# Optimization experiments

Hardware: AMD Instinct MI355X
Metric: run time of the kernel (lower is better)

The kernel has to match this reference:

```python
import jax, jax.numpy as jnp
from jax import lax
import numpy as np
import math

# Static module config (matches init_kwargs)
K = 5            # kernel_size
MD = 3           # max_degree
HH = (MD + 1) ** 2   # n_harmonics = 16
CIN, F = 16, 32
B, D = 1, 48
NJ = K // 2      # n_radial_profiles (one shell per integer radius 1..K//2)
DN = ('NCDHW', 'OIDHW', 'NCDHW')


def _sh_table(ct, st, phi):
    """Complex spherical harmonics Y_n^m up to degree 3 (Condon-Shortley), [*grid, HH]."""
    fourpi = 4.0 * np.pi
    def N(n, m):
        return np.sqrt((2 * n + 1) / fourpi * math.factorial(n - m) / math.factorial(n + m))
    P = {
        (0, 0): np.ones_like(ct),
        (1, 0): ct,
        (1, 1): -st,
        (2, 0): 0.5 * (3 * ct ** 2 - 1),
        (2, 1): -3.0 * ct * st,
        (2, 2): 3.0 * st ** 2,
        (3, 0): 0.5 * (5 * ct ** 3 - 3 * ct),
        (3, 1): -1.5 * (5 * ct ** 2 - 1) * st,
        (3, 2): 15.0 * ct * st ** 2,
        (3, 3): -15.0 * st ** 3,
    }
    sh = np.zeros(ct.shape + (HH,), dtype=np.complex64)
    for n in range(MD + 1):
        for m in range(0, n + 1):
            y = (N(n, m) * P[(n, m)]).astype(np.complex64) * np.exp(1j * m * phi).astype(np.complex64)
            sh[..., n * n + n + m] = y
            if m > 0:
                sh[..., n * n + n - m] = ((-1) ** m) * np.conj(y)
    return sh


def _make_atoms():
    """Radial-shell x SH atoms: [K,K,K,NJ,HH] complex, L2-normalized per atom."""
    g = np.linspace(-(K // 2), K // 2, K)
    x, y, z = np.meshgrid(g, g, g, indexing='xy')
    r = np.sqrt(x * x + y * y + z * z)
    phi = np.arctan2(y, x)
    ct = np.divide(z, r, out=np.zeros_like(r), where=r != 0)
    st = np.sqrt(np.clip(1.0 - ct * ct, 0.0, None))
    sh = _sh_table(ct, st, phi)                                     # [K,K,K,HH]
    prof = np.stack([np.clip(1.0 - np.abs(r - j), 0.0, None) for j in range(1, NJ + 1)], -1)  # [K,K,K,NJ]
    atoms = prof[..., :, None] * sh[..., None, :]                   # [K,K,K,NJ,HH]
    norm = np.sqrt((np.abs(atoms) ** 2).sum(axis=(0, 1, 2), keepdims=True))
    atoms = atoms / np.where(norm > 0, norm, 1.0)
    return atoms.real.astype(np.float32), atoms.imag.astype(np.float32)


ATOMS_R, ATOMS_I = _make_atoms()
DEG = np.repeat(np.arange(MD + 1), 2 * np.arange(MD + 1) + 1)       # harmonic index -> degree (len HH)


def setup_inputs() -> dict:
    key = jax.random.key(0)
    ks = jax.random.split(key, 4)
    lim = float(np.sqrt(6.0 / (CIN + F)))
    return {
        'x': jax.random.normal(ks[0], (B, CIN, D, D, D), jnp.float32),
        'w': jax.random.uniform(ks[1], (CIN, F, NJ, MD + 1), jnp.float32, -lim, lim),
        'central_w': jax.random.uniform(ks[2], (F, CIN, 1, 1, 1), jnp.float32, -lim, lim),
        'central_b': jnp.zeros((F,), jnp.float32),
        'spec_bias': jnp.zeros(((MD + 1) * F,), jnp.float32),
        'proj_w': jax.random.uniform(ks[3], (F, (MD + 1) * F, 1, 1, 1), jnp.float32, -0.1, 0.1),
        'proj_b': jnp.zeros((F,), jnp.float32),
    }


def _forward(x, w, central_w, central_b, spec_bias, proj_w, proj_b):
    # Expand per-degree weights to per-harmonic (repeat_interleave over 2n+1 orders),
    # then fuse the per-channel SH conv + channel/radial weighted sum into a single
    # dense conv with composed kernels (same math as the torch loop + sum over axes 4,6).
    wh = w[..., DEG]                                                 # [C,F,NJ,HH]
    kr = jnp.einsum('cfjh,xyzjh->fhcxyz', wh, jnp.asarray(ATOMS_R)).reshape(F * HH, CIN, K, K, K)
    ki = jnp.einsum('cfjh,xyzjh->fhcxyz', wh, jnp.asarray(ATOMS_I)).reshape(F * HH, CIN, K, K, K)
    yr = lax.conv_general_dilated(x, kr, (1, 1, 1), 'SAME', dimension_numbers=DN)
    yi = lax.conv_general_dilated(x, ki, (1, 1, 1), 'SAME', dimension_numbers=DN)
    b, _, d, h, wd = yr.shape
    yr = yr.reshape(b, F, HH, d, h, wd)
    yi = yi.reshape(b, F, HH, d, h, wd)
    # 1x1x1 central-pixel conv added to the degree-0 (harmonic 0) real map
    cp = lax.conv_general_dilated(x, central_w, (1, 1, 1), 'SAME', dimension_numbers=DN)
    cp = cp + central_b[None, :, None, None, None]
    yr = yr.at[:, :, 0].add(cp)
    # rotation-invariant power spectrum per degree: 1/(2n+1) * sum_m (re^2 + im^2)
    p = yr * yr + yi * yi                                            # [B,F,HH,d,h,w]
    spec = jnp.stack([p[:, :, n * n:n * n + 2 * n + 1].sum(2) / (2 * n + 1) for n in range(MD + 1)], 2)
    spec = spec.reshape(b, F * (MD + 1), d, h, wd) + spec_bias[None, :, None, None, None]
    # activation=('Linear',...) is identity; projection 1x1x1 conv + ReLU
    out = lax.conv_general_dilated(spec, proj_w, (1, 1, 1), 'SAME', dimension_numbers=DN)
    out = out + proj_b[None, :, None, None, None]
    return jax.nn.relu(out)


def reference(x, w, central_w, central_b, spec_bias, proj_w, proj_b):
    return _forward(x, w, central_w, central_b, spec_bias, proj_w, proj_b)
```

## Files before the change

### kernel.cpp

```cpp
#include <hip/hip_runtime.h>
#include <hip/hip_fp16.h>
#include <math.h>


#define TX 8
#define TY 4
#define TZ 4
#define LXX 12
#define LYY 8
#define LZZ 8
#define NPOS 768
#define CPAD 24
#define POSB 48

#define ATAB2_B 0
#define WT2_B   23552
#define CW2_B   31744
#define PWT_B   32768
#define OB_B    49152
#define ED_B    49280

typedef __half2 h2;
union I4H { int4 v; h2 h[4]; };

__global__ __launch_bounds__(256) void ssh_init(
    const float* __restrict__ w, const float* __restrict__ cw,
    const float* __restrict__ proj_w, const float* __restrict__ spec_bias,
    const float* __restrict__ proj_b, char* __restrict__ wsb)
{
    __shared__ float shr[125][16];
    __shared__ float shi[125][16];
    __shared__ float prof[125][2];
    __shared__ float norms[2][16];
    __shared__ int epos[92];
    const int tid = threadIdx.x;
    const float fourpi = 4.0f * 3.14159265358979323846f;

    for (int p = tid; p < 125; p += 256) {
        int d2 = p % 5, d1 = (p / 5) % 5, d0 = p / 25;
        float xc = (float)(d1 - 2), yc = (float)(d0 - 2), zc = (float)(d2 - 2);
        float r2 = xc*xc + yc*yc + zc*zc;
        float r  = sqrtf(r2);
        float phi = atan2f(yc, xc);
        float ct = (r > 0.f) ? (zc / r) : 0.f;
        float st = sqrtf(fmaxf(0.f, 1.f - ct*ct));
        float c1 = cosf(phi), s1 = sinf(phi);
        float c2 = c1*c1 - s1*s1, s2 = 2.f*s1*c1;
        float c3 = c2*c1 - s2*s1, s3 = s2*c1 + c2*s1;
        float P10 = ct,              P11 = -st;
        float P20 = 0.5f*(3.f*ct*ct - 1.f), P21 = -3.f*ct*st, P22 = 3.f*st*st;
        float P30 = 0.5f*(5.f*ct*ct*ct - 3.f*ct);
        float P31 = -1.5f*(5.f*ct*ct - 1.f)*st;
        float P32 = 15.f*ct*st*st;
        float P33 = -15.f*st*st*st;
        float N00 = sqrtf(1.f/fourpi);
        float N10 = sqrtf(3.f/fourpi);
        float N11 = sqrtf(3.f/fourpi * 0.5f);
        float N20 = sqrtf(5.f/fourpi);
        float N21 = sqrtf(5.f/fourpi / 6.f);
        float N22 = sqrtf(5.f/fourpi / 24.f);
        float N30 = sqrtf(7.f/fourpi);
        float N31 = sqrtf(7.f/fourpi / 12.f);
        float N32 = sqrtf(7.f/fourpi / 120.f);
        float N33 = sqrtf(7.f/fourpi / 720.f);
        float b;
        shr[p][0] = N00;               shi[p][0] = 0.f;
        shr[p][2] = N10*P10;           shi[p][2] = 0.f;
        b = N11*P11;
        shr[p][3] =  b*c1;             shi[p][3] =  b*s1;
        shr[p][1] = -b*c1;             shi[p][1] =  b*s1;
        shr[p][6] = N20*P20;           shi[p][6] = 0.f;
        b = N21*P21;
        shr[p][7] =  b*c1;             shi[p][7] =  b*s1;
        shr[p][5] = -b*c1;             shi[p][5] =  b*s1;
        b = N22*P22;
        shr[p][8] =  b*c2;             shi[p][8] =  b*s2;
        shr[p][4] =  b*c2;             shi[p][4] = -b*s2;
        shr[p][12] = N30*P30;          shi[p][12] = 0.f;
        b = N31*P31;
        shr[p][13] =  b*c1;            shi[p][13] =  b*s1;
        shr[p][11] = -b*c1;            shi[p][11] =  b*s1;
        b = N32*P32;
        shr[p][14] =  b*c2;            shi[p][14] =  b*s2;
        shr[p][10] =  b*c2;            shi[p][10] = -b*s2;
        b = N33*P33;
        shr[p][15] =  b*c3;            shi[p][15] =  b*s3;
        shr[p][9]  = -b*c3;            shi[p][9]  =  b*s3;
        prof[p][0] = fmaxf(0.f, 1.f - fabsf(r - 1.f));
        prof[p][1] = fmaxf(0.f, 1.f - fabsf(r - 2.f));
    }
    __syncthreads();

    if (tid < 32) {
        int j = tid >> 4, h = tid & 15;
        float acc = 0.f;
        for (int p = 0; p < 125; ++p) {
            float pr = prof[p][j];
            acc += pr*pr*(shr[p][h]*shr[p][h] + shi[p][h]*shi[p][h]);
        }
        float nn = sqrtf(acc);
        norms[j][h] = (nn > 0.f) ? nn : 1.f;
    }
    if (tid < 125) {
        int p = tid;
        int d2 = p % 5, d1 = (p / 5) % 5, d0 = p / 25;
        int ix = d1 - 2, iy = d0 - 2, iz = d2 - 2;
        int r2i = ix*ix + iy*iy + iz*iz;
        int cls = (r2i == 1) ? 0 : (r2i == 2 || r2i == 3) ? 1
                : (r2i == 4 || r2i == 5 || r2i == 6 || r2i == 8) ? 2 : -1;
        if (cls >= 0) {
            int rank = (cls == 0) ? 0 : (cls == 1) ? 6 : 26;
            for (int q = 0; q < p; ++q) {
                int e2 = q % 5, e1 = (q / 5) % 5, e0 = q / 25;
                int jx = e1 - 2, jy = e0 - 2, jz = e2 - 2;
                int s2i = jx*jx + jy*jy + jz*jz;
                int c2i = (s2i == 1) ? 0 : (s2i == 2 || s2i == 3) ? 1
                       : (s2i == 4 || s2i == 5 || s2i == 6 || s2i == 8) ? 2 : -1;
                rank += (c2i == cls) ? 1 : 0;
            }
            epos[rank] = p;
            ((int*)(wsb + ED_B))[rank] = (d0*(LYY*LXX) + d1*LXX + d2) * POSB;
        }
    }
    __syncthreads();

    h2* at2 = (h2*)(wsb + ATAB2_B);
    for (int t = tid; t < 92*16; t += 256) {
        int e = t >> 4, h = t & 15;
        int p = epos[e];
        float c0 = prof[p][0] / norms[0][h];
        float c1v = prof[p][1] / norms[1][h];
        at2[(h*92+e)*4 + 0] = __float2half2_rn(c0*shr[p][h]);
        at2[(h*92+e)*4 + 1] = __float2half2_rn(c0*shi[p][h]);
        at2[(h*92+e)*4 + 2] = __float2half2_rn(c1v*shr[p][h]);
        at2[(h*92+e)*4 + 3] = __float2half2_rn(c1v*shi[p][h]);
    }
    h2* wt2h = (h2*)(wsb + WT2_B);
    for (int t = tid; t < 2048; t += 256) {
        int n = t >> 9, f = (t >> 4) & 31, j = (t >> 3) & 1, cp = t & 7;
        float a = w[((2*cp*32 + f)*2 + j)*4 + n];
        float b = w[(((2*cp+1)*32 + f)*2 + j)*4 + n];
        wt2h[t] = __halves2half2(__float2half(a), __float2half(b));
    }
    h2* cw2h = (h2*)(wsb + CW2_B);
    for (int t = tid; t < 256; t += 256) {
        int f = t >> 3, cp = t & 7;
        cw2h[t] = __halves2half2(__float2half(cw[f*16 + 2*cp]),
                                 __float2half(cw[f*16 + 2*cp + 1]));
    }
    float* pwT = (float*)(wsb + PWT_B);
    for (int t = tid; t < 4096; t += 256) {
        int i = t >> 5, fo = t & 31;
        pwT[t] = proj_w[fo*128 + i];
    }
    if (tid < 32) {
        float acc = proj_b[tid];
        for (int i = 0; i < 128; ++i) acc += proj_w[tid*128 + i] * spec_bias[i];
        ((float*)(wsb + OB_B))[tid] = acc;
    }
}


__device__ __forceinline__ void conv2c(const __half* __restrict__ ldsh, int baseb,
    const int4* __restrict__ aA, const int4* __restrict__ aB,
    const int* __restrict__ ed, h2 (&zA)[4][8], h2 (&zB)[4][8])
{
#pragma unroll
    for (int r = 0; r < 4; ++r)
#pragma unroll
        for (int q = 0; q < 8; ++q) { zA[r][q] = __float2half2_rn(0.f); zB[r][q] = __float2half2_rn(0.f); }

#pragma unroll 2
    for (int e = 0; e < 6; ++e) {
        I4H ca, cb_, x0, x1;
        ca.v = aA[e]; cb_.v = aB[e];
        const int4* p = (const int4*)((const char*)ldsh + baseb + ed[e]);
        x0.v = p[0]; x1.v = p[1];
#pragma unroll
        for (int q = 0; q < 4; ++q) {
            zA[0][q]   = __hfma2(ca.h[0],  x0.h[q], zA[0][q]);
            zA[1][q]   = __hfma2(ca.h[1],  x0.h[q], zA[1][q]);
            zB[0][q]   = __hfma2(cb_.h[0], x0.h[q], zB[0][q]);
            zB[1][q]   = __hfma2(cb_.h[1], x0.h[q], zB[1][q]);
            zA[0][q+4] = __hfma2(ca.h[0],  x1.h[q], zA[0][q+4]);
            zA[1][q+4] = __hfma2(ca.h[1],  x1.h[q], zA[1][q+4]);
            zB[0][q+4] = __hfma2(cb_.h[0], x1.h[q], zB[0][q+4]);
            zB[1][q+4] = __hfma2(cb_.h[1], x1.h[q], zB[1][q+4]);
        }
    }
#pragma unroll 2
    for (int e = 6; e < 26; ++e) {
        I4H ca, cb_, x0, x1;
        ca.v = aA[e]; cb_.v = aB[e];
        const int4* p = (const int4*)((const char*)ldsh + baseb + ed[e]);
        x0.v = p[0]; x1.v = p[1];
#pragma unroll
        for (int q = 0; q < 4; ++q) {
            zA[0][q]   = __hfma2(ca.h[0],  x0.h[q], zA[0][q]);
            zA[1][q]   = __hfma2(ca.h[1],  x0.h[q], zA[1][q]);
            zA[2][q]   = __hfma2(ca.h[2],  x0.h[q], zA[2][q]);
            zA[3][q]   = __hfma2(ca.h[3],  x0.h[q], zA[3][q]);
            zB[0][q]   = __hfma2(cb_.h[0], x0.h[q], zB[0][q]);
            zB[1][q]   = __hfma2(cb_.h[1], x0.h[q], zB[1][q]);
            zB[2][q]   = __hfma2(cb_.h[2], x0.h[q], zB[2][q]);
            zB[3][q]   = __hfma2(cb_.h[3], x0.h[q], zB[3][q]);
            zA[0][q+4] = __hfma2(ca.h[0],  x1.h[q], zA[0][q+4]);
            zA[1][q+4] = __hfma2(ca.h[1],  x1.h[q], zA[1][q+4]);
            zA[2][q+4] = __hfma2(ca.h[2],  x1.h[q], zA[2][q+4]);
            zA[3][q+4] = __hfma2(ca.h[3],  x1.h[q], zA[3][q+4]);
            zB[0][q+4] = __hfma2(cb_.h[0], x1.h[q], zB[0][q+4]);
            zB[1][q+4] = __hfma2(cb_.h[1], x1.h[q], zB[1][q+4]);
            zB[2][q+4] = __hfma2(cb_.h[2], x1.h[q], zB[2][q+4]);
            zB[3][q+4] = __hfma2(cb_.h[3], x1.h[q], zB[3][q+4]);
        }
    }
#pragma unroll 2
    for (int e = 26; e < 92; ++e) {
        I4H ca, cb_, x0, x1;
        ca.v = aA[e]; cb_.v = aB[e];
        const int4* p = (const int4*)((const char*)ldsh + baseb + ed[e]);
        x0.v = p[0]; x1.v = p[1];
#pragma unroll
        for (int q = 0; q < 4; ++q) {
            zA[2][q]   = __hfma2(ca.h[2],  x0.h[q], zA[2][q]);
            zA[3][q]   = __hfma2(ca.h[3],  x0.h[q], zA[3][q]);
            zB[2][q]   = __hfma2(cb_.h[2], x0.h[q], zB[2][q]);
            zB[3][q]   = __hfma2(cb_.h[3], x0.h[q], zB[3][q]);
            zA[2][q+4] = __hfma2(ca.h[2],  x1.h[q], zA[2][q+4]);
            zA[3][q+4] = __hfma2(ca.h[3],  x1.h[q], zA[3][q+4]);
            zB[2][q+4] = __hfma2(cb_.h[2], x1.h[q], zB[2][q+4]);
            zB[3][q+4] = __hfma2(cb_.h[3], x1.h[q], zB[3][q+4]);
        }
    }
}

__device__ __forceinline__ void conv1c(const __half* __restrict__ ldsh, int baseb,
    const int4* __restrict__ aA, const int* __restrict__ ed, h2 (&zA)[4][8])
{
#pragma unroll
    for (int r = 0; r < 4; ++r)
#pragma unroll
        for (int q = 0; q < 8; ++q) zA[r][q] = __float2half2_rn(0.f);

#pragma unroll 2
    for (int e = 0; e < 6; ++e) {
        I4H ca, x0, x1;
        ca.v = aA[e];
        const int4* p = (const int4*)((const char*)ldsh + baseb + ed[e]);
        x0.v = p[0]; x1.v = p[1];
#pragma unroll
        for (int q = 0; q < 4; ++q) {
            zA[0][q]   = __hfma2(ca.h[0], x0.h[q], zA[0][q]);
            zA[1][q]   = __hfma2(ca.h[1], x0.h[q], zA[1][q]);
            zA[0][q+4] = __hfma2(ca.h[0], x1.h[q], zA[0][q+4]);
            zA[1][q+4] = __hfma2(ca.h[1], x1.h[q], zA[1][q+4]);
        }
    }
#pragma unroll 2
    for (int e = 6; e < 26; ++e) {
        I4H ca, x0, x1;
        ca.v = aA[e];
        const int4* p = (const int4*)((const char*)ldsh + baseb + ed[e]);
        x0.v = p[0]; x1.v = p[1];
#pragma unroll
        for (int q = 0; q < 4; ++q) {
            zA[0][q]   = __hfma2(ca.h[0], x0.h[q], zA[0][q]);
            zA[1][q]   = __hfma2(ca.h[1], x0.h[q], zA[1][q]);
            zA[2][q]   = __hfma2(ca.h[2], x0.h[q], zA[2][q]);
            zA[3][q]   = __hfma2(ca.h[3], x0.h[q], zA[3][q]);
            zA[0][q+4] = __hfma2(ca.h[0], x1.h[q], zA[0][q+4]);
            zA[1][q+4] = __hfma2(ca.h[1], x1.h[q], zA[1][q+4]);
            zA[2][q+4] = __hfma2(ca.h[2], x1.h[q], zA[2][q+4]);
            zA[3][q+4] = __hfma2(ca.h[3], x1.h[q], zA[3][q+4]);
        }
    }
#pragma unroll 2
    for (int e = 26; e < 92; ++e) {
        I4H ca, x0, x1;
        ca.v = aA[e];
        const int4* p = (const int4*)((const char*)ldsh + baseb + ed[e]);
        x0.v = p[0]; x1.v = p[1];
#pragma unroll
        for (int q = 0; q < 4; ++q) {
            zA[2][q]   = __hfma2(ca.h[2], x0.h[q], zA[2][q]);
            zA[3][q]   = __hfma2(ca.h[3], x0.h[q], zA[3][q]);
            zA[2][q+4] = __hfma2(ca.h[2], x1.h[q], zA[2][q+4]);
            zA[3][q+4] = __hfma2(ca.h[3], x1.h[q], zA[3][q+4]);
        }
    }
}

__device__ __forceinline__ void conv2r(const __half* __restrict__ ldsh, int baseb,
    const int4* __restrict__ aA, const int4* __restrict__ aB,
    const int* __restrict__ ed, h2 (&z)[4][8])
{
#pragma unroll
    for (int r = 0; r < 4; ++r)
#pragma unroll
        for (int q = 0; q < 8; ++q) z[r][q] = __float2half2_rn(0.f);

#pragma unroll 2
    for (int e = 0; e < 6; ++e) {
        I4H ca, cb_, x0, x1;
        ca.v = aA[e]; cb_.v = aB[e];
        const int4* p = (const int4*)((const char*)ldsh + baseb + ed[e]);
        x0.v = p[0]; x1.v = p[1];
#pragma unroll
        for (int q = 0; q < 4; ++q) {
            z[0][q]   = __hfma2(ca.h[0],  x0.h[q], z[0][q]);
            z[2][q]   = __hfma2(cb_.h[0], x0.h[q], z[2][q]);
            z[0][q+4] = __hfma2(ca.h[0],  x1.h[q], z[0][q+4]);
            z[2][q+4] = __hfma2(cb_.h[0], x1.h[q], z[2][q+4]);
        }
    }
#pragma unroll 2
    for (int e = 6; e < 26; ++e) {
        I4H ca, cb_, x0, x1;
        ca.v = aA[e]; cb_.v = aB[e];
        const int4* p = (const int4*)((const char*)ldsh + baseb + ed[e]);
        x0.v = p[0]; x1.v = p[1];
#pragma unroll
        for (int q = 0; q < 4; ++q) {
            z[0][q]   = __hfma2(ca.h[0],  x0.h[q], z[0][q]);
            z[1][q]   = __hfma2(ca.h[2],  x0.h[q], z[1][q]);
            z[2][q]   = __hfma2(cb_.h[0], x0.h[q], z[2][q]);
            z[3][q]   = __hfma2(cb_.h[2], x0.h[q], z[3][q]);
            z[0][q+4] = __hfma2(ca.h[0],  x1.h[q], z[0][q+4]);
            z[1][q+4] = __hfma2(ca.h[2],  x1.h[q], z[1][q+4]);
            z[2][q+4] = __hfma2(cb_.h[0], x1.h[q], z[2][q+4]);
            z[3][q+4] = __hfma2(cb_.h[2], x1.h[q], z[3][q+4]);
        }
    }
#pragma unroll 2
    for (int e = 26; e < 92; ++e) {
        I4H ca, cb_, x0, x1;
        ca.v = aA[e]; cb_.v = aB[e];
        const int4* p = (const int4*)((const char*)ldsh + baseb + ed[e]);
        x0.v = p[0]; x1.v = p[1];
#pragma unroll
        for (int q = 0; q < 4; ++q) {
            z[1][q]   = __hfma2(ca.h[2],  x0.h[q], z[1][q]);
            z[3][q]   = __hfma2(cb_.h[2], x0.h[q], z[3][q]);
            z[1][q+4] = __hfma2(ca.h[2],  x1.h[q], z[1][q+4]);
            z[3][q+4] = __hfma2(cb_.h[2], x1.h[q], z[3][q+4]);
        }
    }
}


template<int N>
__device__ __forceinline__ void mixc(const h2 (&z)[4][8],
    const int4* __restrict__ wt2n, const float* __restrict__ pwT, float2 (&outa)[16])
{
    const float W = 2.f / (float)(2*N + 1);
#pragma unroll 2
    for (int f = 0; f < 32; ++f) {
        I4H w00, w01, w10, w11;
        w00.v = wt2n[f*4+0]; w01.v = wt2n[f*4+1];
        w10.v = wt2n[f*4+2]; w11.v = wt2n[f*4+3];
        h2 yr = __float2half2_rn(0.f), yi = __float2half2_rn(0.f);
#pragma unroll
        for (int q = 0; q < 4; ++q) {
            yr = __hfma2(w00.h[q], z[0][q],   yr);
            yr = __hfma2(w01.h[q], z[0][q+4], yr);
            yr = __hfma2(w10.h[q], z[2][q],   yr);
            yr = __hfma2(w11.h[q], z[2][q+4], yr);
            yi = __hfma2(w00.h[q], z[1][q],   yi);
            yi = __hfma2(w01.h[q], z[1][q+4], yi);
            yi = __hfma2(w10.h[q], z[3][q],   yi);
            yi = __hfma2(w11.h[q], z[3][q+4], yi);
        }
        float yrf = __low2float(yr) + __high2float(yr);
        float yif = __low2float(yi) + __high2float(yi);
        float s = (yrf*yrf + yif*yif) * W;
        const float2* pw2 = (const float2*)(pwT + (f*4 + N)*32);
#pragma unroll
        for (int k = 0; k < 16; ++k) {
            float2 t = pw2[k];
            outa[k].x = fmaf(t.x, s, outa[k].x);
            outa[k].y = fmaf(t.y, s, outa[k].y);
        }
    }
}

template<int R, int N, bool CENTRAL>
__device__ __forceinline__ void mixr(const h2 (&z)[4][8],
    const int4* __restrict__ wt2n, const int4* __restrict__ cw2,
    const float* __restrict__ cbp, const __half* __restrict__ ldsh, int baseb,
    const float* __restrict__ pwT, float2 (&outa)[16])
{
    const float W = 1.f / (float)(2*N + 1);
    h2 xc[8];
    if (CENTRAL) {
        const int4* pc = (const int4*)((const char*)ldsh + baseb + 218*POSB);
        I4H xc0, xc1; xc0.v = pc[0]; xc1.v = pc[1];
#pragma unroll
        for (int q = 0; q < 4; ++q) { xc[q] = xc0.h[q]; xc[q+4] = xc1.h[q]; }
    }
#pragma unroll 2
    for (int f = 0; f < 32; ++f) {
        I4H w00, w01, w10, w11;
        w00.v = wt2n[f*4+0]; w01.v = wt2n[f*4+1];
        w10.v = wt2n[f*4+2]; w11.v = wt2n[f*4+3];
        h2 yr = __float2half2_rn(0.f);
#pragma unroll
        for (int q = 0; q < 4; ++q) {
            yr = __hfma2(w00.h[q], z[R][q],     yr);
            yr = __hfma2(w01.h[q], z[R][q+4],   yr);
            yr = __hfma2(w10.h[q], z[R+1][q],   yr);
            yr = __hfma2(w11.h[q], z[R+1][q+4], yr);
        }
        float yrf = __low2float(yr) + __high2float(yr);
        if (CENTRAL) {
            I4H c0, c1; c0.v = cw2[f*2]; c1.v = cw2[f*2+1];
            h2 acc = __float2half2_rn(0.f);
#pragma unroll
            for (int q = 0; q < 4; ++q) {
                acc = __hfma2(c0.h[q], xc[q],   acc);
                acc = __hfma2(c1.h[q], xc[q+4], acc);
            }
            yrf += cbp[f] + __low2float(acc) + __high2float(acc);
        }
        float s = yrf*yrf * W;
        const float2* pw2 = (const float2*)(pwT + (f*4 + N)*32);
#pragma unroll
        for (int k = 0; k < 16; ++k) {
            float2 t = pw2[k];
            outa[k].x = fmaf(t.x, s, outa[k].x);
            outa[k].y = fmaf(t.y, s, outa[k].y);
        }
    }
}

__global__ __launch_bounds__(256, 3) void ssh_main(
    const float* __restrict__ x, const float* __restrict__ cb,
    const char* __restrict__ wsb, float* __restrict__ out)
{
    __shared__ __align__(16) __half ldsh[NPOS * CPAD];
    const int tid = threadIdx.x;
    const int x0 = blockIdx.x * TX, y0 = blockIdx.y * TY, z0 = blockIdx.z * TZ;

    for (int i = tid; i < NPOS * 8; i += 256) {
        int cp = i / NPOS;
        int pos = i - cp * NPOS;
        int lx = pos % LXX; int t1 = pos / LXX;
        int ly = t1 % LYY;  int lz = t1 / LYY;
        int gx = x0 + lx - 2, gy = y0 + ly - 2, gz = z0 + lz - 2;
        h2 hv = __float2half2_rn(0.f);
        if ((unsigned)gx < 48u && (unsigned)gy < 48u && (unsigned)gz < 48u) {
            int gi = ((2*cp*48 + gz)*48 + gy)*48 + gx;
            hv = __floats2half2_rn(x[gi], x[gi + 48*48*48]);
        }
        *(h2*)(ldsh + pos*CPAD + 2*cp) = hv;
    }
    __syncthreads();

    const int hf  = tid >> 7;
    const int vid = tid & 127;
    const int tx = vid & 7, ty = (vid >> 3) & 3, tz = vid >> 5;
    const int baseb = (tz*(LYY*LXX) + ty*LXX + tx) * POSB;

    const int4* __restrict__ atab = (const int4*)(wsb + ATAB2_B);
    const int4* __restrict__ wt2  = (const int4*)(wsb + WT2_B);
    const int4* __restrict__ cw2  = (const int4*)(wsb + CW2_B);
    const float* __restrict__ pwT = (const float*)(wsb + PWT_B);
    const float* __restrict__ obase = (const float*)(wsb + OB_B);
    const int* __restrict__ ed    = (const int*)(wsb + ED_B);

    float2 outa[16];
#pragma unroll
    for (int k = 0; k < 16; ++k) outa[k] = make_float2(0.f, 0.f);

    h2 zA[4][8], zB[4][8];
    if (hf == 0) {
        conv2c(ldsh, baseb, atab + 13*92, atab + 14*92, ed, zA, zB);
        mixc<3>(zA, wt2 + 3*128, pwT, outa);
        mixc<3>(zB, wt2 + 3*128, pwT, outa);
        conv1c(ldsh, baseb, atab + 15*92, ed, zA);
        mixc<3>(zA, wt2 + 3*128, pwT, outa);
        conv2r(ldsh, baseb, atab + 12*92, atab + 0*92, ed, zB);
        mixr<0,3,false>(zB, wt2 + 3*128, cw2, cb, ldsh, baseb, pwT, outa);
        mixr<2,0,true >(zB, wt2 + 0*128, cw2, cb, ldsh, baseb, pwT, outa);
    } else {
        conv2c(ldsh, baseb, atab + 7*92, atab + 8*92, ed, zA, zB);
        mixc<2>(zA, wt2 + 2*128, pwT, outa);
        mixc<2>(zB, wt2 + 2*128, pwT, outa);
        conv2r(ldsh, baseb, atab + 6*92, atab + 2*92, ed, zA);
        mixr<0,2,false>(zA, wt2 + 2*128, cw2, cb, ldsh, baseb, pwT, outa);
        conv1c(ldsh, baseb, atab + 3*92, ed, zB);
        mixc<1>(zB, wt2 + 1*128, pwT, outa);
        mixr<2,1,false>(zA, wt2 + 1*128, cw2, cb, ldsh, baseb, pwT, outa);
    }

    __syncthreads();
    float* lmerge = (float*)ldsh;
    if (hf == 1) {
#pragma unroll
        for (int k = 0; k < 16; ++k) {
            lmerge[vid*33 + 2*k]     = outa[k].x;
            lmerge[vid*33 + 2*k + 1] = outa[k].y;
        }
    }
    __syncthreads();
    if (hf == 0) {
        const int gz = z0 + tz, gy = y0 + ty, gx = x0 + tx;
#pragma unroll
        for (int k = 0; k < 16; ++k) {
            float v0 = obase[2*k]   + outa[k].x + lmerge[vid*33 + 2*k];
            float v1 = obase[2*k+1] + outa[k].y + lmerge[vid*33 + 2*k + 1];
            out[(((2*k)*48   + gz)*48 + gy)*48 + gx] = fmaxf(v0, 0.f);
            out[(((2*k+1)*48 + gz)*48 + gy)*48 + gx] = fmaxf(v1, 0.f);
        }
    }
}

extern "C" void kernel_launch(void* const* d_in, const int* in_sizes, int n_in,
                              void* d_out, int out_size, void* d_ws, size_t ws_size,
                              hipStream_t stream) {
    const float* x  = (const float*)d_in[0];
    const float* w  = (const float*)d_in[1];
    const float* cw = (const float*)d_in[2];
    const float* cb = (const float*)d_in[3];
    const float* sb = (const float*)d_in[4];
    const float* pw = (const float*)d_in[5];
    const float* pb = (const float*)d_in[6];
    float* out = (float*)d_out;
    char* wsb = (char*)d_ws;

    ssh_init<<<dim3(1), dim3(256), 0, stream>>>(w, cw, pw, sb, pb, wsb);
    ssh_main<<<dim3(48/TX, 48/TY, 48/TZ), dim3(256), 0, stream>>>(x, cb, wsb, out);
}
```

Baseline: 169.8 us.

## Fuse same-degree mix passes so projection accumulates once per degree

Merges the per-harmonic projection passes that share a degree (two complex maps, or a complex plus a real map) into one loop over output channels. The squared magnitudes are summed before a single 16-wide projection update. This drops the repeated weight loads and outa FMA sweeps, and raises the unroll factors of the tap loops in the conv helpers. The cost is higher register pressure from keeping more accumulators live at once, which could hurt occupancy or cause spills.

Measured after the change: 160.3 us. -5.6%, faster.

```diff
diff --git a/kernel.cpp b/kernel.cpp
--- a/kernel.cpp
+++ b/kernel.cpp
@@ -170,7 +170,7 @@
 #pragma unroll
         for (int q = 0; q < 8; ++q) { zA[r][q] = __float2half2_rn(0.f); zB[r][q] = __float2half2_rn(0.f); }
 
-#pragma unroll 2
+#pragma unroll 3
     for (int e = 0; e < 6; ++e) {
         I4H ca, cb_, x0, x1;
         ca.v = aA[e]; cb_.v = aB[e];
@@ -188,7 +188,7 @@
             zB[1][q+4] = __hfma2(cb_.h[1], x1.h[q], zB[1][q+4]);
         }
     }
-#pragma unroll 2
+#pragma unroll 4
     for (int e = 6; e < 26; ++e) {
         I4H ca, cb_, x0, x1;
         ca.v = aA[e]; cb_.v = aB[e];
@@ -214,7 +214,7 @@
             zB[3][q+4] = __hfma2(cb_.h[3], x1.h[q], zB[3][q+4]);
         }
     }
-#pragma unroll 2
+#pragma unroll 3
     for (int e = 26; e < 92; ++e) {
         I4H ca, cb_, x0, x1;
         ca.v = aA[e]; cb_.v = aB[e];
@@ -242,7 +242,7 @@
 #pragma unroll
         for (int q = 0; q < 8; ++q) zA[r][q] = __float2half2_rn(0.f);
 
-#pragma unroll 2
+#pragma unroll 3
     for (int e = 0; e < 6; ++e) {
         I4H ca, x0, x1;
         ca.v = aA[e];
@@ -256,7 +256,7 @@
             zA[1][q+4] = __hfma2(ca.h[1], x1.h[q], zA[1][q+4]);
         }
     }
-#pragma unroll 2
+#pragma unroll 4
     for (int e = 6; e < 26; ++e) {
         I4H ca, x0, x1;
         ca.v = aA[e];
@@ -274,7 +274,7 @@
             zA[3][q+4] = __hfma2(ca.h[3], x1.h[q], zA[3][q+4]);
         }
     }
-#pragma unroll 2
+#pragma unroll 3
     for (int e = 26; e < 92; ++e) {
         I4H ca, x0, x1;
         ca.v = aA[e];
@@ -299,7 +299,7 @@
 #pragma unroll
         for (int q = 0; q < 8; ++q) z[r][q] = __float2half2_rn(0.f);
 
-#pragma unroll 2
+#pragma unroll 3
     for (int e = 0; e < 6; ++e) {
         I4H ca, cb_, x0, x1;
         ca.v = aA[e]; cb_.v = aB[e];
@@ -313,7 +313,7 @@
             z[2][q+4] = __hfma2(cb_.h[0], x1.h[q], z[2][q+4]);
         }
     }
-#pragma unroll 2
+#pragma unroll 4
     for (int e = 6; e < 26; ++e) {
         I4H ca, cb_, x0, x1;
         ca.v = aA[e]; cb_.v = aB[e];
@@ -331,7 +331,7 @@
             z[3][q+4] = __hfma2(cb_.h[2], x1.h[q], z[3][q+4]);
         }
     }
-#pragma unroll 2
+#pragma unroll 3
     for (int e = 26; e < 92; ++e) {
         I4H ca, cb_, x0, x1;
         ca.v = aA[e]; cb_.v = aB[e];
@@ -348,8 +348,10 @@
 }
 
 
+#define CDEL (2*(LYY*LXX) + 2*LXX + 2)
+
 template<int N>
-__device__ __forceinline__ void mixc(const h2 (&z)[4][8],
+__device__ __forceinline__ void mixc2(const h2 (&zA)[4][8], const h2 (&zB)[4][8],
     const int4* __restrict__ wt2n, const float* __restrict__ pwT, float2 (&outa)[16])
 {
     const float W = 2.f / (float)(2*N + 1);
@@ -358,21 +360,74 @@
         I4H w00, w01, w10, w11;
         w00.v = wt2n[f*4+0]; w01.v = wt2n[f*4+1];
         w10.v = wt2n[f*4+2]; w11.v = wt2n[f*4+3];
+        h2 yrA = __float2half2_rn(0.f), yiA = __float2half2_rn(0.f);
+        h2 yrB = __float2half2_rn(0.f), yiB = __float2half2_rn(0.f);
+#pragma unroll
+        for (int q = 0; q < 4; ++q) {
+            yrA = __hfma2(w00.h[q], zA[0][q],   yrA);
+            yrA = __hfma2(w01.h[q], zA[0][q+4], yrA);
+            yrA = __hfma2(w10.h[q], zA[2][q],   yrA);
+            yrA = __hfma2(w11.h[q], zA[2][q+4], yrA);
+            yiA = __hfma2(w00.h[q], zA[1][q],   yiA);
+            yiA = __hfma2(w01.h[q], zA[1][q+4], yiA);
+            yiA = __hfma2(w10.h[q], zA[3][q],   yiA);
+            yiA = __hfma2(w11.h[q], zA[3][q+4], yiA);
+            yrB = __hfma2(w00.h[q], zB[0][q],   yrB);
+            yrB = __hfma2(w01.h[q], zB[0][q+4], yrB);
+            yrB = __hfma2(w10.h[q], zB[2][q],   yrB);
+            yrB = __hfma2(w11.h[q], zB[2][q+4], yrB);
+            yiB = __hfma2(w00.h[q], zB[1][q],   yiB);
+            yiB = __hfma2(w01.h[q], zB[1][q+4], yiB);
+            yiB = __hfma2(w10.h[q], zB[3][q],   yiB);
+            yiB = __hfma2(w11.h[q], zB[3][q+4], yiB);
+        }
+        float ra = __low2float(yrA) + __high2float(yrA);
+        float ia = __low2float(yiA) + __high2float(yiA);
+        float rb = __low2float(yrB) + __high2float(yrB);
+        float ib = __low2float(yiB) + __high2float(yiB);
+        float s = (ra*ra + ia*ia + rb*rb + ib*ib) * W;
+        const float2* pw2 = (const float2*)(pwT + (f*4 + N)*32);
+#pragma unroll
+        for (int k = 0; k < 16; ++k) {
+            float2 t = pw2[k];
+            outa[k].x = fmaf(t.x, s, outa[k].x);
+            outa[k].y = fmaf(t.y, s, outa[k].y);
+        }
+    }
+}
+
+template<int RR, int N>
+__device__ __forceinline__ void mix_cr(const h2 (&zC)[4][8], const h2 (&zR)[4][8],
+    const int4* __restrict__ wt2n, const float* __restrict__ pwT, float2 (&outa)[16])
+{
+    const float Wc = 2.f / (float)(2*N + 1);
+    const float Wr = 1.f / (float)(2*N + 1);
+#pragma unroll 2
+    for (int f = 0; f < 32; ++f) {
+        I4H w00, w01, w10, w11;
+        w00.v = wt2n[f*4+0]; w01.v = wt2n[f*4+1];
+        w10.v = wt2n[f*4+2]; w11.v = wt2n[f*4+3];
         h2 yr = __float2half2_rn(0.f), yi = __float2half2_rn(0.f);
-#pragma unroll
-        for (int q = 0; q < 4; ++q) {
-            yr = __hfma2(w00.h[q], z[0][q],   yr);
-            yr = __hfma2(w01.h[q], z[0][q+4], yr);
-            yr = __hfma2(w10.h[q], z[2][q],   yr);
-            yr = __hfma2(w11.h[q], z[2][q+4], yr);
-            yi = __hfma2(w00.h[q], z[1][q],   yi);
-            yi = __hfma2(w01.h[q], z[1][q+4], yi);
-            yi = __hfma2(w10.h[q], z[3][q],   yi);
-            yi = __hfma2(w11.h[q], z[3][q+4], yi);
-        }
-        float yrf = __low2float(yr) + __high2float(yr);
-        float yif = __low2float(yi) + __high2float(yi);
-        float s = (yrf*yrf + yif*yif) * W;
+        h2 yR = __float2half2_rn(0.f);
+#pragma unroll
+        for (int q = 0; q < 4; ++q) {
+            yr = __hfma2(w00.h[q], zC[0][q],   yr);
+            yr = __hfma2(w01.h[q], zC[0][q+4], yr);
+            yr = __hfma2(w10.h[q], zC[2][q],   yr);
+            yr = __hfma2(w11.h[q], zC[2][q+4], yr);
+            yi = __hfma2(w00.h[q], zC[1][q],   yi);
+            yi = __hfma2(w01.h[q], zC[1][q+4], yi);
+            yi = __hfma2(w10.h[q], zC[3][q],   yi);
+            yi = __hfma2(w11.h[q], zC[3][q+4], yi);
+            yR = __hfma2(w00.h[q], zR[RR][q],     yR);
+            yR = __hfma2(w01.h[q], zR[RR][q+4],   yR);
+            yR = __hfma2(w10.h[q], zR[RR+1][q],   yR);
+            yR = __hfma2(w11.h[q], zR[RR+1][q+4], yR);
+        }
+        float rc = __low2float(yr) + __high2float(yr);
+        float ic = __low2float(yi) + __high2float(yi);
+        float rr = __low2float(yR) + __high2float(yR);
+        float s = (rc*rc + ic*ic) * Wc + rr*rr * Wr;
         const float2* pw2 = (const float2*)(pwT + (f*4 + N)*32);
 #pragma unroll
         for (int k = 0; k < 16; ++k) {
@@ -392,7 +447,7 @@
     const float W = 1.f / (float)(2*N + 1);
     h2 xc[8];
     if (CENTRAL) {
-        const int4* pc = (const int4*)((const char*)ldsh + baseb + 218*POSB);
+        const int4* pc = (const int4*)((const char*)ldsh + baseb + CDEL*POSB);
         I4H xc0, xc1; xc0.v = pc[0]; xc1.v = pc[1];
 #pragma unroll
         for (int q = 0; q < 4; ++q) { xc[q] = xc0.h[q]; xc[q+4] = xc1.h[q]; }
@@ -461,11 +516,11 @@
     const int baseb = (tz*(LYY*LXX) + ty*LXX + tx) * POSB;
 
     const int4* __restrict__ atab = (const int4*)(wsb + ATAB2_B);
+    const int*  __restrict__ ed   = (const int*)(wsb + ED_B);
     const int4* __restrict__ wt2  = (const int4*)(wsb + WT2_B);
     const int4* __restrict__ cw2  = (const int4*)(wsb + CW2_B);
     const float* __restrict__ pwT = (const float*)(wsb + PWT_B);
     const float* __restrict__ obase = (const float*)(wsb + OB_B);
-    const int* __restrict__ ed    = (const int*)(wsb + ED_B);
 
     float2 outa[16];
 #pragma unroll
@@ -474,22 +529,18 @@
     h2 zA[4][8], zB[4][8];
     if (hf == 0) {
         conv2c(ldsh, baseb, atab + 13*92, atab + 14*92, ed, zA, zB);
-        mixc<3>(zA, wt2 + 3*128, pwT, outa);
-        mixc<3>(zB, wt2 + 3*128, pwT, outa);
+        mixc2<3>(zA, zB, wt2 + 3*128, pwT, outa);
         conv1c(ldsh, baseb, atab + 15*92, ed, zA);
-        mixc<3>(zA, wt2 + 3*128, pwT, outa);
         conv2r(ldsh, baseb, atab + 12*92, atab + 0*92, ed, zB);
-        mixr<0,3,false>(zB, wt2 + 3*128, cw2, cb, ldsh, baseb, pwT, outa);
-        mixr<2,0,true >(zB, wt2 + 0*128, cw2, cb, ldsh, baseb, pwT, outa);
+        mix_cr<0,3>(zA, zB, wt2 + 3*128, pwT, outa);
+        mixr<2,0,true>(zB, wt2 + 0*128, cw2, cb, ldsh, baseb, pwT, outa);
     } else {
         conv2c(ldsh, baseb, atab + 7*92, atab + 8*92, ed, zA, zB);
-        mixc<2>(zA, wt2 + 2*128, pwT, outa);
-        mixc<2>(zB, wt2 + 2*128, pwT, outa);
+        mixc2<2>(zA, zB, wt2 + 2*128, pwT, outa);
         conv2r(ldsh, baseb, atab + 6*92, atab + 2*92, ed, zA);
+        conv1c(ldsh, baseb, atab + 3*92, ed, zB);
+        mix_cr<2,1>(zB, zA, wt2 + 1*128, pwT, outa);
         mixr<0,2,false>(zA, wt2 + 2*128, cw2, cb, ldsh, baseb, pwT, outa);
-        conv1c(ldsh, baseb, atab + 3*92, ed, zB);
-        mixc<1>(zB, wt2 + 1*128, pwT, outa);
-        mixr<2,1,false>(zA, wt2 + 1*128, cw2, cb, ldsh, baseb, pwT, outa);
     }
 
     __syncthreads();
```
